# Kernel tuning notes

Hardware: AMD Instinct MI355X
Metric: run time of the kernel (lower is better)

Reference implementation:

```python
import jax, jax.numpy as jnp
import numpy as np
import math

D_MODEL = 1024
NUM_HEADS = 16
D_K = D_MODEL // NUM_HEADS
B, L = 2, 2048
ROPE_BASE = 10000.0


def _rope_cos_sin(seq_len, dim, dtype=jnp.float32):
    inv_freq = 1.0 / (ROPE_BASE ** (jnp.arange(0, dim, 2, dtype=jnp.float32) / dim))
    t = jnp.arange(seq_len, dtype=jnp.float32)
    freqs = jnp.outer(t, inv_freq)            # [L, dim/2]
    emb = jnp.concatenate([freqs, freqs], -1)  # [L, dim]
    return jnp.cos(emb).astype(dtype), jnp.sin(emb).astype(dtype)


def _apply_rope(x, cos, sin):
    # x: [B, H, L, d_k]; cos/sin: [L, d_k]
    x1, x2 = jnp.split(x, 2, axis=-1)
    rotated = jnp.concatenate([-x2, x1], axis=-1)
    return x * cos + rotated * sin


def setup_inputs() -> dict:
    key = jax.random.key(0)
    ks = jax.random.split(key, 12)
    s = 1.0 / math.sqrt(D_MODEL)
    inp = {
        "query": jax.random.normal(ks[0], (B, L, D_MODEL), jnp.float32),
        "key":   jax.random.normal(ks[1], (B, L, D_MODEL), jnp.float32),
        "value": jax.random.normal(ks[2], (B, L, D_MODEL), jnp.float32),
        "mask":  jnp.triu(jnp.ones((L, L), jnp.bool_), k=1)[None, None],  # causal, True = masked
        "Wq": jax.random.uniform(ks[3], (D_MODEL, D_MODEL), jnp.float32, -s, s),
        "bq": jnp.zeros((D_MODEL,), jnp.float32),
        "Wk": jax.random.uniform(ks[4], (D_MODEL, D_MODEL), jnp.float32, -s, s),
        "bk": jnp.zeros((D_MODEL,), jnp.float32),
        "Wv": jax.random.uniform(ks[5], (D_MODEL, D_MODEL), jnp.float32, -s, s),
        "bv": jnp.zeros((D_MODEL,), jnp.float32),
        "Wo": jax.random.uniform(ks[6], (D_MODEL, D_MODEL), jnp.float32, -s, s),
        "bo": jnp.zeros((D_MODEL,), jnp.float32),
    }
    return inp


def reference(query, key, value, mask, Wq, bq, Wk, bk, Wv, bv, Wo, bo):
    b, l, _ = query.shape
    def proj(x, W, bias):
        return (x @ W.T + bias).reshape(b, l, NUM_HEADS, D_K).transpose(0, 2, 1, 3)
    q = proj(query, Wq, bq)   # [B, H, L, d_k]
    k = proj(key,   Wk, bk)
    v = proj(value, Wv, bv)
    cos, sin = _rope_cos_sin(l, D_K, q.dtype)
    q = _apply_rope(q, cos, sin)
    k = _apply_rope(k, cos, sin)
    scale = 1.0 / math.sqrt(D_K)
    att = jnp.einsum('bhqd,bhkd->bhqk', q, k) * scale
    att = jnp.where(mask, jnp.finfo(att.dtype).min, att)
    att = jax.nn.softmax(att, axis=-1)
    out = jnp.einsum('bhqk,bhkd->bhqd', att, v)
    out = out.transpose(0, 2, 1, 3).reshape(b, l, D_MODEL)
    return out @ Wo.T + bo
```

## Files before the change

### kernel.cpp

```cpp
#include <hip/hip_runtime.h>
#include <cstdint>

typedef _Float16 half_t;
using half8 = __attribute__((ext_vector_type(8))) half_t;
using half4 = __attribute__((ext_vector_type(4))) half_t;
using f32x4 = __attribute__((ext_vector_type(4))) float;
using f32x16 = __attribute__((ext_vector_type(16))) float;

#define LSEQ 2048
#define DM   1024
#define NH   16
#define DK   64

__device__ inline void gload_lds16(const void* g, void* l) {
    __builtin_amdgcn_global_load_lds(
        (const __attribute__((address_space(1))) uint32_t*)g,
        (__attribute__((address_space(3))) uint32_t*)l, 16, 0, 0);
}

__device__ inline uint32_t pk2(float a, float b) {
    auto h = __builtin_amdgcn_cvt_pkrtz(a, b);
    return __builtin_bit_cast(uint32_t, h);
}

__device__ inline float ex2(float x) { return __builtin_amdgcn_exp2f(x); }

__global__ __launch_bounds__(256) void cvt_kernel(
    const float* __restrict__ q, const float* __restrict__ k, const float* __restrict__ v,
    const float* __restrict__ wq, const float* __restrict__ wk,
    const float* __restrict__ wv, const float* __restrict__ wo,
    half_t* __restrict__ dst)
{
    long tid = (long)blockIdx.x * 256 + threadIdx.x;
    long e = tid * 4;
    const float* src;
    long off;
    if (e < 12582912L) {
        int a = (int)(e >> 22);
        src = (a == 0) ? q : (a == 1) ? k : v;
        off = e & 4194303L;
    } else {
        long ew = e - 12582912L;
        int w = (int)(ew >> 20);
        src = (w == 0) ? wq : (w == 1) ? wk : (w == 2) ? wv : wo;
        off = ew & 1048575L;
    }
    float4 x = *(const float4*)(src + off);
    half4 o;
    o[0] = (half_t)x.x; o[1] = (half_t)x.y; o[2] = (half_t)x.z; o[3] = (half_t)x.w;
    *(half4*)(dst + e) = o;
}

__global__ __launch_bounds__(256) void rope_tab(float* __restrict__ cosT, float* __restrict__ sinT) {
    int tid = blockIdx.x * 256 + threadIdx.x;
    int j = tid >> 11;
    int pos = tid & 2047;
    float invf = powf(10000.0f, -(float)j / 32.0f);
    float a = (float)pos * invf;
    cosT[tid] = cosf(a);
    sinT[tid] = sinf(a);
}

__global__ __launch_bounds__(512, 6) void qkv_gemm(
    const half_t* __restrict__ XH, const half_t* __restrict__ WH,
    const float* __restrict__ bq, const float* __restrict__ bk, const float* __restrict__ bv,
    half_t* __restrict__ QF, half_t* __restrict__ KF, half_t* __restrict__ VF,
    const float* __restrict__ cosT, const float* __restrict__ sinT)
{
    __shared__ alignas(16) unsigned short sA[2][128 * 32];
    __shared__ alignas(16) unsigned short sB[2][128 * 32];
    const int mode = blockIdx.z;
    const half_t* A  = XH + (long)mode * 4194304L;
    const half_t* Bw = WH + (long)mode * 1048576L;
    const float* bias = (mode == 0) ? bq : (mode == 1) ? bk : bv;

    const int tid = threadIdx.x;
    const int lane = tid & 63, wid = tid >> 6;
    const int g = lane >> 4, c = lane & 15;
    const int wr = wid >> 1, wc = wid & 1;
    const int row0 = blockIdx.y * 128, col0 = blockIdx.x * 128;

    f32x4 acc[2][4] = {};
    const int srow = lane >> 2;
    const int scol = ((lane & 3) ^ ((lane >> 3) & 3)) * 8;
    const int kx   = (g ^ ((c >> 1) & 3)) * 8;

    auto stage = [&](int buf, int k0) {
        int r = wid * 16;
        gload_lds16(A  + (long)(row0 + r + srow) * DM + k0 + scol, &sA[buf][r * 32]);
        gload_lds16(Bw + (long)(col0 + r + srow) * DM + k0 + scol, &sB[buf][r * 32]);
    };

    stage(0, 0);
    __syncthreads();
    int cur = 0;
#pragma unroll 1
    for (int k0 = 0; k0 < DM; k0 += 32) {
        if (k0 + 32 < DM) stage(cur ^ 1, k0 + 32);
        half8 af[2], bf[4];
#pragma unroll
        for (int m = 0; m < 2; ++m)
            af[m] = *(const half8*)&sA[cur][(wr * 32 + m * 16 + c) * 32 + kx];
#pragma unroll
        for (int n = 0; n < 4; ++n)
            bf[n] = *(const half8*)&sB[cur][(wc * 64 + n * 16 + c) * 32 + kx];
#pragma unroll
        for (int m = 0; m < 2; ++m)
#pragma unroll
            for (int n = 0; n < 4; ++n)
                acc[m][n] = __builtin_amdgcn_mfma_f32_16x16x32_f16(af[m], bf[n], acc[m][n], 0, 0, 0);
        __syncthreads();
        cur ^= 1;
    }

    if (mode == 2) {
        const int h = blockIdx.x * 2 + wc;
#pragma unroll
        for (int n = 0; n < 4; ++n) {
            int col = col0 + wc * 64 + n * 16 + c;
            int d = n * 16 + c;
            float bvv = bias[col];
#pragma unroll
            for (int m = 0; m < 2; ++m) {
                int row = row0 + wr * 32 + m * 16 + g * 4;
                int b = row >> 11, pos = row & 2047;
                int bh = b * NH + h;
                long idx = (((((long)bh * 32 + (pos >> 6)) * 2 + (d >> 5)) * 4
                             + ((pos >> 4) & 3)) * 64
                            + (((pos >> 3) & 1) * 32 + (d & 31))) * 8 + (pos & 7);
                half4 o;
#pragma unroll
                for (int r = 0; r < 4; ++r) o[r] = (half_t)(acc[m][n][r] + bvv);
                *(half4*)(VF + idx) = o;
            }
        }
    } else {
        const float SC = (mode == 0) ? 0.125f * 1.44269504f : 1.0f;
        half_t* OF = (mode == 0) ? QF : KF;
#pragma unroll
        for (int np = 0; np < 2; ++np) {
            int col1 = col0 + wc * 64 + np * 16 + c;
            int h = col1 >> 6;
            int d1 = np * 16 + c;
            float b1 = bias[col1], b2 = bias[col1 + 32];
            const float* Cp = cosT + d1 * 2048;
            const float* Sp = sinT + d1 * 2048;
#pragma unroll
            for (int m = 0; m < 2; ++m) {
                int row = row0 + wr * 32 + m * 16 + g * 4;
                int pos0 = row & 2047;
                float4 cv4 = *(const float4*)(Cp + pos0);
                float4 sv4 = *(const float4*)(Sp + pos0);
#pragma unroll
                for (int r = 0; r < 4; ++r) {
                    int pos = pos0 + r;
                    int b = (row + r) >> 11;
                    int bh = b * NH + h;
                    float cv = ((const float*)&cv4)[r];
                    float sv = ((const float*)&sv4)[r];
                    float x1 = acc[m][np][r] + b1;
                    float x2 = acc[m][np + 2][r] + b2;
                    long kbase = ((long)(bh * 64 + (pos >> 5)) * 4) * 512
                               + ((c >> 3) * 32 + (pos & 31)) * 8 + (c & 7);
                    OF[kbase + (long)np * 512]       = (half_t)((x1 * cv - x2 * sv) * SC);
                    OF[kbase + (long)(np + 2) * 512] = (half_t)((x2 * cv + x1 * sv) * SC);
                }
            }
        }
    }
}

__global__ __launch_bounds__(512, 4) void out_gemm(
    const half_t* __restrict__ A, const half_t* __restrict__ Bw,
    const float* __restrict__ bias, float* __restrict__ o32)
{
    __shared__ alignas(16) unsigned short sA[2][128 * 32];
    __shared__ alignas(16) unsigned short sB[2][64 * 32];
    const int tid = threadIdx.x;
    const int lane = tid & 63, wid = tid >> 6;
    const int g = lane >> 4, c = lane & 15;
    const int wr = wid >> 1, wc = wid & 1;
    const int row0 = blockIdx.y * 128, col0 = blockIdx.x * 64;

    f32x4 acc[2][2] = {};
    const int srow = lane >> 2;
    const int scol = ((lane & 3) ^ ((lane >> 3) & 3)) * 8;
    const int kx   = (g ^ ((c >> 1) & 3)) * 8;

    auto stage = [&](int buf, int k0) {
        int rA = wid * 16;
        gload_lds16(A + (long)(row0 + rA + srow) * DM + k0 + scol, &sA[buf][rA * 32]);
        if (wid < 4) {
            int rB = wid * 16;
            gload_lds16(Bw + (long)(col0 + rB + srow) * DM + k0 + scol, &sB[buf][rB * 32]);
        }
    };

    stage(0, 0);
    __syncthreads();
    int cur = 0;
#pragma unroll 1
    for (int k0 = 0; k0 < DM; k0 += 32) {
        if (k0 + 32 < DM) stage(cur ^ 1, k0 + 32);
        half8 af[2], bf[2];
#pragma unroll
        for (int m = 0; m < 2; ++m)
            af[m] = *(const half8*)&sA[cur][(wr * 32 + m * 16 + c) * 32 + kx];
#pragma unroll
        for (int n = 0; n < 2; ++n)
            bf[n] = *(const half8*)&sB[cur][(wc * 32 + n * 16 + c) * 32 + kx];
#pragma unroll
        for (int m = 0; m < 2; ++m)
#pragma unroll
            for (int n = 0; n < 2; ++n)
                acc[m][n] = __builtin_amdgcn_mfma_f32_16x16x32_f16(af[m], bf[n], acc[m][n], 0, 0, 0);
        __syncthreads();
        cur ^= 1;
    }
#pragma unroll
    for (int n = 0; n < 2; ++n) {
        int col = col0 + wc * 32 + n * 16 + c;
        float bv = bias[col];
#pragma unroll
        for (int m = 0; m < 2; ++m)
#pragma unroll
            for (int r = 0; r < 4; ++r) {
                int row = row0 + wr * 32 + m * 16 + g * 4 + r;
                o32[(long)row * DM + col] = acc[m][n][r] + bv;
            }
    }
}

__global__ __launch_bounds__(512, 2) void attn_k(
    const half_t* __restrict__ QF, const half_t* __restrict__ KF,
    const half_t* __restrict__ VF, half_t* __restrict__ AO)
{
    __shared__ half_t sK[2 * 4096];
    __shared__ half_t sV[2 * 4096];

    const int tid = threadIdx.x;
    const int lane = tid & 63, wid = tid >> 6;
    const int pr = blockIdx.x >> 5;
    const int bh = blockIdx.x & 31;
    const int qc = lane & 31, hi = lane >> 5;
    const int b = bh >> 4, h = bh & 15;
    const int lo8 = lane * 8;
    const int sub = wid & 3, grp = wid >> 2;

    const half_t* QU = QF + (long)bh * 131072;
    const half_t* KU = KF + (long)bh * 131072;
    const half_t* VU = VF + (long)bh * 131072;

    const int t1 = 15 - pr;
    const int t  = grp ? pr : t1;
    const int qb = 128 * t + 32 * sub;
    const int kend = qb + 32;
    const int kmax = 128 * t1 + 128;

    half8 qf[4];
#pragma unroll
    for (int dc = 0; dc < 4; ++dc)
        qf[dc] = *(const half8*)(QU + (qb >> 5) * 2048 + dc * 512 + lo8);

    f32x16 acc[2] = {};
    float lp[16];
#pragma unroll
    for (int r = 0; r < 16; ++r) lp[r] = 0.0f;
    float m = -INFINITY;

    union PB { uint32_t u[4]; half8 h8; };

    auto stage = [&](int buf, int k0) {
        gload_lds16(KU + (long)k0 * 64 + wid * 512 + lo8, sK + buf * 4096 + wid * 512);
        gload_lds16(VU + (long)k0 * 64 + wid * 512 + lo8, sV + buf * 4096 + wid * 512);
    };

    stage(0, 0);
    __syncthreads();

    int cur = 0;
#pragma unroll 1
    for (int k0 = 0; k0 < kmax; k0 += 64) {
        int kn = k0 + 64;
        if (kn < kmax) stage(cur ^ 1, kn);

        if (k0 < kend) {
            const half_t* bK = sK + cur * 4096;
            const half_t* bV = sV + cur * 4096;
            half8 kf0[4], kf1[4], vf[2][4];
#pragma unroll
            for (int dc = 0; dc < 4; ++dc) {
                kf0[dc] = *(const half8*)(bK + dc * 512 + lo8);
                kf1[dc] = *(const half8*)(bK + 2048 + dc * 512 + lo8);
            }
#pragma unroll
            for (int dt = 0; dt < 2; ++dt)
#pragma unroll
                for (int kc = 0; kc < 4; ++kc)
                    vf[dt][kc] = *(const half8*)(bV + (dt * 4 + kc) * 512 + lo8);

            f32x16 s0 = {}, s1 = {};
            __builtin_amdgcn_s_setprio(1);
#pragma unroll
            for (int dc = 0; dc < 4; ++dc) s0 = __builtin_amdgcn_mfma_f32_32x32x16_f16(kf0[dc], qf[dc], s0, 0, 0, 0);
#pragma unroll
            for (int dc = 0; dc < 4; ++dc) s1 = __builtin_amdgcn_mfma_f32_32x32x16_f16(kf1[dc], qf[dc], s1, 0, 0, 0);
            __builtin_amdgcn_s_setprio(0);

            if (kn >= kend) {
                int qg = qb + qc;
#pragma unroll
                for (int r = 0; r < 16; ++r) {
                    int crow = (r & 3) + 8 * (r >> 2) + 4 * hi;
                    if (k0 + crow > qg)      s0[r] = -INFINITY;
                    if (k0 + 32 + crow > qg) s1[r] = -INFINITY;
                }
            }

            float mx[8];
#pragma unroll
            for (int r = 0; r < 8; ++r)
                mx[r] = fmaxf(fmaxf(s0[r], s0[8 + r]), fmaxf(s1[r], s1[8 + r]));
#pragma unroll
            for (int st = 4; st >= 1; st >>= 1)
#pragma unroll
                for (int r = 0; r < 4; ++r)
                    if (r < st) mx[r] = fmaxf(mx[r], mx[r + st]);
            float pm = fmaxf(mx[0], __shfl_xor(mx[0], 32, 64));
            if (__any(pm > m + 8.0f)) {
                float mn = fmaxf(m, pm);
                float sc = ex2(m - mn);
#pragma unroll
                for (int r = 0; r < 16; ++r) {
                    acc[0][r] *= sc; acc[1][r] *= sc; lp[r] *= sc;
                }
                m = mn;
            }
#pragma unroll
            for (int r = 0; r < 16; ++r) {
                s0[r] = ex2(s0[r] - m);
                s1[r] = ex2(s1[r] - m);
                lp[r] += s0[r] + s1[r];
            }

            uint32_t A0[8], A1[8];
#pragma unroll
            for (int i = 0; i < 8; ++i) {
                A0[i] = pk2(s0[2 * i], s0[2 * i + 1]);
                A1[i] = pk2(s1[2 * i], s1[2 * i + 1]);
            }
            PB B00, B01, B10, B11;
            {
                auto r0 = __builtin_amdgcn_permlane32_swap(A0[0], A0[2], false, false);
                B00.u[0] = r0[0]; B00.u[2] = r0[1];
                auto r1 = __builtin_amdgcn_permlane32_swap(A0[1], A0[3], false, false);
                B00.u[1] = r1[0]; B00.u[3] = r1[1];
                auto r2 = __builtin_amdgcn_permlane32_swap(A0[4], A0[6], false, false);
                B01.u[0] = r2[0]; B01.u[2] = r2[1];
                auto r3 = __builtin_amdgcn_permlane32_swap(A0[5], A0[7], false, false);
                B01.u[1] = r3[0]; B01.u[3] = r3[1];
                auto r4 = __builtin_amdgcn_permlane32_swap(A1[0], A1[2], false, false);
                B10.u[0] = r4[0]; B10.u[2] = r4[1];
                auto r5 = __builtin_amdgcn_permlane32_swap(A1[1], A1[3], false, false);
                B10.u[1] = r5[0]; B10.u[3] = r5[1];
                auto r6 = __builtin_amdgcn_permlane32_swap(A1[4], A1[6], false, false);
                B11.u[0] = r6[0]; B11.u[2] = r6[1];
                auto r7 = __builtin_amdgcn_permlane32_swap(A1[5], A1[7], false, false);
                B11.u[1] = r7[0]; B11.u[3] = r7[1];
            }

            __builtin_amdgcn_s_setprio(1);
#pragma unroll
            for (int dt = 0; dt < 2; ++dt) {
                acc[dt] = __builtin_amdgcn_mfma_f32_32x32x16_f16(vf[dt][0], B00.h8, acc[dt], 0, 0, 0);
                acc[dt] = __builtin_amdgcn_mfma_f32_32x32x16_f16(vf[dt][1], B01.h8, acc[dt], 0, 0, 0);
                acc[dt] = __builtin_amdgcn_mfma_f32_32x32x16_f16(vf[dt][2], B10.h8, acc[dt], 0, 0, 0);
                acc[dt] = __builtin_amdgcn_mfma_f32_32x32x16_f16(vf[dt][3], B11.h8, acc[dt], 0, 0, 0);
            }
            __builtin_amdgcn_s_setprio(0);
        }
        __syncthreads();
        cur ^= 1;
    }

    float ls = lp[0];
#pragma unroll
    for (int r = 1; r < 16; ++r) ls += lp[r];
    float l = ls + __shfl_xor(ls, 32, 64);
    float inv = 1.0f / l;
    long obase = ((long)(b * LSEQ + qb + qc)) * DM + h * 64;
#pragma unroll
    for (int dt = 0; dt < 2; ++dt)
#pragma unroll
        for (int rg = 0; rg < 4; ++rg) {
            half4 o;
#pragma unroll
            for (int e = 0; e < 4; ++e) o[e] = (half_t)(acc[dt][4 * rg + e] * inv);
            *(half4*)(AO + obase + dt * 32 + 8 * rg + 4 * hi) = o;
        }
}

extern "C" void kernel_launch(void* const* d_in, const int* in_sizes, int n_in,
                              void* d_out, int out_size, void* d_ws, size_t ws_size,
                              hipStream_t stream) {
    const float* q  = (const float*)d_in[0];
    const float* k  = (const float*)d_in[1];
    const float* v  = (const float*)d_in[2];
    const float* wq = (const float*)d_in[4];
    const float* bq = (const float*)d_in[5];
    const float* wk = (const float*)d_in[6];
    const float* bk = (const float*)d_in[7];
    const float* wv = (const float*)d_in[8];
    const float* bv = (const float*)d_in[9];
    const float* wo = (const float*)d_in[10];
    const float* bo = (const float*)d_in[11];

    uint8_t* wsb = (uint8_t*)d_ws;
    half_t* XH = (half_t*)wsb;
    half_t* WH = XH + 12582912L;
    float*  COS = (float*)(wsb + 33554432L);
    float*  SIN = (float*)(wsb + 33816576L);
    half_t* QF = (half_t*)(wsb + 34078720L);
    half_t* KF = (half_t*)(wsb + 42467328L);
    half_t* VF = (half_t*)(wsb + 50855936L);
    half_t* AO = (half_t*)(wsb + 59244544L);

    cvt_kernel<<<16384, 256, 0, stream>>>(q, k, v, wq, wk, wv, wo, XH);
    rope_tab<<<256, 256, 0, stream>>>(COS, SIN);

    qkv_gemm<<<dim3(8, 32, 3), 512, 0, stream>>>(XH, WH, bq, bk, bv, QF, KF, VF, COS, SIN);

    attn_k<<<256, 512, 0, stream>>>(QF, KF, VF, AO);

    out_gemm<<<dim3(16, 32), 512, 0, stream>>>(AO, WH + 3145728L, bo, (float*)d_out);
}
```

Measured before the change: 121.9 us.

## Split attention KV range across warp groups and fuse rope table into convert

The attention kernel no longer pairs a short and a long causal query tile per block. Each block now handles one 128-row query tile, and its two warp groups process alternating 64-key halves of each 128-key stage. Their partial softmax states (max, sum, output) are merged through shared memory at the end, and the grid doubles to 512 blocks with occupancy hint 3. Separately, the rope table computation is folded into extra blocks of the conversion kernel, which removes one launch. The change trades a larger LDS footprint and an extra merge step for less per-block serial work and more parallelism, but causal work now varies more across blocks.

Result: faster. 116.4 us (median of 4 runs) (-4.5%).

```diff
diff --git a/kernel.cpp b/kernel.cpp
--- a/kernel.cpp
+++ b/kernel.cpp
@@ -29,8 +29,18 @@
     const float* __restrict__ q, const float* __restrict__ k, const float* __restrict__ v,
     const float* __restrict__ wq, const float* __restrict__ wk,
     const float* __restrict__ wv, const float* __restrict__ wo,
-    half_t* __restrict__ dst)
+    half_t* __restrict__ dst, float* __restrict__ cosT, float* __restrict__ sinT)
 {
+    if (blockIdx.x >= 16384) {
+        int tid = (blockIdx.x - 16384) * 256 + threadIdx.x;
+        int j = tid >> 11;
+        int pos = tid & 2047;
+        float invf = powf(10000.0f, -(float)j / 32.0f);
+        float a = (float)pos * invf;
+        cosT[tid] = cosf(a);
+        sinT[tid] = sinf(a);
+        return;
+    }
     long tid = (long)blockIdx.x * 256 + threadIdx.x;
     long e = tid * 4;
     const float* src;
@@ -51,16 +61,6 @@
     *(half4*)(dst + e) = o;
 }
 
-__global__ __launch_bounds__(256) void rope_tab(float* __restrict__ cosT, float* __restrict__ sinT) {
-    int tid = blockIdx.x * 256 + threadIdx.x;
-    int j = tid >> 11;
-    int pos = tid & 2047;
-    float invf = powf(10000.0f, -(float)j / 32.0f);
-    float a = (float)pos * invf;
-    cosT[tid] = cosf(a);
-    sinT[tid] = sinf(a);
-}
-
 __global__ __launch_bounds__(512, 6) void qkv_gemm(
     const half_t* __restrict__ XH, const half_t* __restrict__ WH,
     const float* __restrict__ bq, const float* __restrict__ bk, const float* __restrict__ bv,
@@ -231,16 +231,16 @@
     }
 }
 
-__global__ __launch_bounds__(512, 2) void attn_k(
+__global__ __launch_bounds__(512, 3) void attn_k(
     const half_t* __restrict__ QF, const half_t* __restrict__ KF,
     const half_t* __restrict__ VF, half_t* __restrict__ AO)
 {
-    __shared__ half_t sK[2 * 4096];
-    __shared__ half_t sV[2 * 4096];
+    __shared__ half_t sK[2 * 8192];
+    __shared__ half_t sV[2 * 8192];
 
     const int tid = threadIdx.x;
     const int lane = tid & 63, wid = tid >> 6;
-    const int pr = blockIdx.x >> 5;
+    const int t  = 15 - (blockIdx.x >> 5);
     const int bh = blockIdx.x & 31;
     const int qc = lane & 31, hi = lane >> 5;
     const int b = bh >> 4, h = bh & 15;
@@ -251,11 +251,8 @@
     const half_t* KU = KF + (long)bh * 131072;
     const half_t* VU = VF + (long)bh * 131072;
 
-    const int t1 = 15 - pr;
-    const int t  = grp ? pr : t1;
     const int qb = 128 * t + 32 * sub;
     const int kend = qb + 32;
-    const int kmax = 128 * t1 + 128;
 
     half8 qf[4];
 #pragma unroll
@@ -271,22 +268,26 @@
     union PB { uint32_t u[4]; half8 h8; };
 
     auto stage = [&](int buf, int k0) {
-        gload_lds16(KU + (long)k0 * 64 + wid * 512 + lo8, sK + buf * 4096 + wid * 512);
-        gload_lds16(VU + (long)k0 * 64 + wid * 512 + lo8, sV + buf * 4096 + wid * 512);
+#pragma unroll
+        for (int rr = 0; rr < 2; ++rr) {
+            gload_lds16(KU + (long)k0 * 64 + rr * 4096 + wid * 512 + lo8,
+                        sK + buf * 8192 + rr * 4096 + wid * 512);
+            gload_lds16(VU + (long)k0 * 64 + rr * 4096 + wid * 512 + lo8,
+                        sV + buf * 8192 + rr * 4096 + wid * 512);
+        }
     };
 
+    const int nit = t + 1;
     stage(0, 0);
     __syncthreads();
-
     int cur = 0;
 #pragma unroll 1
-    for (int k0 = 0; k0 < kmax; k0 += 64) {
-        int kn = k0 + 64;
-        if (kn < kmax) stage(cur ^ 1, kn);
-
-        if (k0 < kend) {
-            const half_t* bK = sK + cur * 4096;
-            const half_t* bV = sV + cur * 4096;
+    for (int i = 0; i < nit; ++i) {
+        if (i + 1 < nit) stage(cur ^ 1, 128 * (i + 1));
+        const int base = 128 * i + grp * 64;
+        if (base < kend) {
+            const half_t* bK = sK + cur * 8192 + grp * 4096;
+            const half_t* bV = sV + cur * 8192 + grp * 4096;
             half8 kf0[4], kf1[4], vf[2][4];
 #pragma unroll
             for (int dc = 0; dc < 4; ++dc) {
@@ -307,13 +308,13 @@
             for (int dc = 0; dc < 4; ++dc) s1 = __builtin_amdgcn_mfma_f32_32x32x16_f16(kf1[dc], qf[dc], s1, 0, 0, 0);
             __builtin_amdgcn_s_setprio(0);
 
-            if (kn >= kend) {
+            if (base + 64 >= kend) {
                 int qg = qb + qc;
 #pragma unroll
                 for (int r = 0; r < 16; ++r) {
                     int crow = (r & 3) + 8 * (r >> 2) + 4 * hi;
-                    if (k0 + crow > qg)      s0[r] = -INFINITY;
-                    if (k0 + 32 + crow > qg) s1[r] = -INFINITY;
+                    if (base + crow > qg)      s0[r] = -INFINITY;
+                    if (base + 32 + crow > qg) s1[r] = -INFINITY;
                 }
             }
 
@@ -345,9 +346,9 @@
 
             uint32_t A0[8], A1[8];
 #pragma unroll
-            for (int i = 0; i < 8; ++i) {
-                A0[i] = pk2(s0[2 * i], s0[2 * i + 1]);
-                A1[i] = pk2(s1[2 * i], s1[2 * i + 1]);
+            for (int i2 = 0; i2 < 8; ++i2) {
+                A0[i2] = pk2(s0[2 * i2], s0[2 * i2 + 1]);
+                A1[i2] = pk2(s1[2 * i2], s1[2 * i2 + 1]);
             }
             PB B00, B01, B10, B11;
             {
@@ -386,18 +387,44 @@
     float ls = lp[0];
 #pragma unroll
     for (int r = 1; r < 16; ++r) ls += lp[r];
-    float l = ls + __shfl_xor(ls, 32, 64);
-    float inv = 1.0f / l;
-    long obase = ((long)(b * LSEQ + qb + qc)) * DM + h * 64;
-#pragma unroll
-    for (int dt = 0; dt < 2; ++dt)
-#pragma unroll
-        for (int rg = 0; rg < 4; ++rg) {
-            half4 o;
-#pragma unroll
-            for (int e = 0; e < 4; ++e) o[e] = (half_t)(acc[dt][4 * rg + e] * inv);
-            *(half4*)(AO + obase + dt * 32 + 8 * rg + 4 * hi) = o;
-        }
+
+    float* mA  = (float*)sK;
+    float* mML = (float*)sV;
+    if (grp == 1) {
+        float* p = mA + sub * 2048;
+#pragma unroll
+        for (int dt = 0; dt < 2; ++dt)
+#pragma unroll
+            for (int r = 0; r < 16; ++r)
+                p[(dt * 16 + r) * 64 + lane] = acc[dt][r];
+        mML[sub * 128 + lane] = m;
+        mML[sub * 128 + 64 + lane] = ls;
+    }
+    __syncthreads();
+    if (grp == 0) {
+        float m1  = mML[sub * 128 + lane];
+        float ls1 = mML[sub * 128 + 64 + lane];
+        float M = fmaxf(m, m1);
+        float e0 = ex2(m - M), e1 = ex2(m1 - M);
+        float lsM = ls * e0 + ls1 * e1;
+        float l = lsM + __shfl_xor(lsM, 32, 64);
+        float inv = 1.0f / l;
+        const float* p = mA + sub * 2048;
+        long obase = ((long)(b * LSEQ + qb + qc)) * DM + h * 64;
+#pragma unroll
+        for (int dt = 0; dt < 2; ++dt)
+#pragma unroll
+            for (int rg = 0; rg < 4; ++rg) {
+                half4 o;
+#pragma unroll
+                for (int e = 0; e < 4; ++e) {
+                    int r = 4 * rg + e;
+                    float Ov = acc[dt][r] * e0 + p[(dt * 16 + r) * 64 + lane] * e1;
+                    o[e] = (half_t)(Ov * inv);
+                }
+                *(half4*)(AO + obase + dt * 32 + 8 * rg + 4 * hi) = o;
+            }
+    }
 }
 
 extern "C" void kernel_launch(void* const* d_in, const int* in_sizes, int n_in,
@@ -425,12 +452,11 @@
     half_t* VF = (half_t*)(wsb + 50855936L);
     half_t* AO = (half_t*)(wsb + 59244544L);
 
-    cvt_kernel<<<16384, 256, 0, stream>>>(q, k, v, wq, wk, wv, wo, XH);
-    rope_tab<<<256, 256, 0, stream>>>(COS, SIN);
+    cvt_kernel<<<16640, 256, 0, stream>>>(q, k, v, wq, wk, wv, wo, XH, COS, SIN);
 
     qkv_gemm<<<dim3(8, 32, 3), 512, 0, stream>>>(XH, WH, bq, bk, bv, QF, KF, VF, COS, SIN);
 
-    attn_k<<<256, 512, 0, stream>>>(QF, KF, VF, AO);
+    attn_k<<<512, 512, 0, stream>>>(QF, KF, VF, AO);
 
     out_gemm<<<dim3(16, 32), 512, 0, stream>>>(AO, WH + 3145728L, bo, (float*)d_out);
 }
```
